# Kernel optimization log

Measured on AMD Instinct MI355X. Metric: run time of the kernel, lower is better.

## Reference

```python
import jax, jax.numpy as jnp
import numpy as np

RADIUS = 4
SIGMA_1 = 5.0
SIGMA_2 = 1.0


def _gaussian_kernel(dtype):
    # norm.pdf(d)/norm.pdf(0) == exp(-d^2/2)
    x2 = jnp.linspace(-RADIUS, RADIUS, 2 * RADIUS + 1) ** 2
    dist = jnp.sqrt(x2[:, None] + x2[None, :]) / SIGMA_1
    return jnp.exp(-0.5 * dist ** 2).astype(dtype)  # [k, k]


def setup_inputs() -> dict:
    key = jax.random.key(0)
    k1, k2 = jax.random.split(key)
    labels = jax.random.uniform(k1, (16, 20, 256, 256), dtype=jnp.float32)
    inputs = jax.random.uniform(k2, (16, 3, 256, 256), dtype=jnp.float32)
    return {"labels": labels, "inputs": inputs}


def reference(labels, inputs):
    B, K, H, W = labels.shape
    kernel = _gaussian_kernel(labels.dtype)

    # per-class mean color: mean(inputs * probs, HW) / (mean(probs, HW) + 1e-5)
    pmean = jnp.mean(labels, axis=(2, 3))                           # [B, K]
    xmean = jnp.einsum('bchw,bkhw->bkc', inputs, labels) / (H * W)  # [B, K, C]
    class_mean = xmean / (pmean[..., None] + 1e-5)                  # [B, K, C]

    # diff = sum_c (x_c - m_c)^2, expanded to avoid a [B,K,C,H,W] intermediate
    x2sum = jnp.sum(inputs ** 2, axis=1)                            # [B, H, W]
    cross = jnp.einsum('bchw,bkc->bkhw', inputs, class_mean)        # [B, K, H, W]
    m2 = jnp.sum(class_mean ** 2, axis=-1)                          # [B, K]
    diff = x2sum[:, None] - 2.0 * cross + m2[:, :, None, None]      # [B, K, H, W]
    weights = jnp.exp(-(diff ** 2) / (SIGMA_2 ** 2))                # [B, K, H, W]

    def blur(x):  # single-channel gaussian conv, vectorized over B*K
        lhs = x.reshape(B * K, 1, H, W)
        rhs = kernel[None, None]  # [1, 1, k, k]
        y = jax.lax.conv_general_dilated(
            lhs, rhs, window_strides=(1, 1),
            padding=[(RADIUS, RADIUS), (RADIUS, RADIUS)],
            dimension_numbers=('NCHW', 'OIHW', 'NCHW'))
        return y.reshape(B, K, H, W)

    num = jnp.sum(labels * blur(labels * weights), axis=(0, 2, 3))  # [K]
    den = jnp.sum(labels * blur(weights), axis=(0, 2, 3))           # [K]
    loss = jnp.sum(jnp.abs(num / (den + 1e-6)))
    return jnp.asarray(K, labels.dtype) - loss
```

## Files before the change

kernel.cpp:

```cpp
#include <hip/hip_runtime.h>

#define B_ 16
#define K_ 20
#define H_ 256
#define W_ 256
#define HW_ (H_*W_)
#define BK_ (B_*K_)
#define TH_ 64
#define BATCH_ 8
#define KT_ 10
#define SCH_ 16
#define NBLK_FUSED_ (4*K_*B_)

#define WS_ND_   (SCH_*4*BK_)
#define WS_CNT_  (WS_ND_ + 2*NBLK_FUSED_)

#define G1T 0.980198673f
#define G2T 0.923116346f
#define G3T 0.835270211f
#define G4T 0.726149037f

__device__ __forceinline__ float rfl(float v) {
    return __int_as_float(__builtin_amdgcn_readfirstlane(__float_as_int(v)));
}

__global__ __launch_bounds__(256) void stats_k(const float* __restrict__ labels,
                                               const float* __restrict__ inputs,
                                               float* __restrict__ ws) {
    const int x = threadIdx.x;
    const int chunk = blockIdx.x;
    const int kt = blockIdx.y;
    const int b  = blockIdx.z;
    const int k0 = kt * KT_;
    if (chunk == 0 && kt == 0 && b == 0 && x == 0)
        ((unsigned*)(ws + WS_CNT_))[0] = 0u;

    const int cbase = chunk * (16 * W_ / 4);
    const float4* in0 = (const float4*)inputs + (size_t)b * 3 * (HW_/4) + cbase;
    const float4* in1 = in0 + (HW_/4);
    const float4* in2 = in1 + (HW_/4);
    const float4* lb  = (const float4*)labels + (size_t)(b * K_ + k0) * (HW_/4) + cbase;

    float acc[KT_][4];
#pragma unroll
    for (int kk = 0; kk < KT_; ++kk)
        acc[kk][0] = acc[kk][1] = acc[kk][2] = acc[kk][3] = 0.f;

#pragma unroll
    for (int it = 0; it < 4; ++it) {
        const int idx = it * 256 + x;
        const float4 a0 = in0[idx];
        const float4 a1 = in1[idx];
        const float4 a2 = in2[idx];
#pragma unroll
        for (int kk = 0; kk < KT_; ++kk) {
            const float4 l = lb[kk * (HW_/4) + idx];
            acc[kk][0] += (l.x + l.y) + (l.z + l.w);
            acc[kk][1] += fmaf(l.w, a0.w, fmaf(l.z, a0.z, fmaf(l.y, a0.y, l.x * a0.x)));
            acc[kk][2] += fmaf(l.w, a1.w, fmaf(l.z, a1.z, fmaf(l.y, a1.y, l.x * a1.x)));
            acc[kk][3] += fmaf(l.w, a2.w, fmaf(l.z, a2.z, fmaf(l.y, a2.y, l.x * a2.x)));
        }
    }

#pragma unroll
    for (int kk = 0; kk < KT_; ++kk)
#pragma unroll
        for (int q = 0; q < 4; ++q)
            for (int o = 32; o > 0; o >>= 1)
                acc[kk][q] += __shfl_down(acc[kk][q], o);

    __shared__ float sred[4][KT_][4];
    const int widx = x >> 6, lane = x & 63;
    if (lane == 0)
#pragma unroll
        for (int kk = 0; kk < KT_; ++kk)
#pragma unroll
            for (int q = 0; q < 4; ++q) sred[widx][kk][q] = acc[kk][q];
    __syncthreads();
    if (x < KT_ * 4) {
        const int kk = x >> 2, q = x & 3;
        const float v = sred[0][kk][q] + sred[1][kk][q] + sred[2][kk][q] + sred[3][kk][q];
        ws[(chunk * 4 + q) * BK_ + b * K_ + k0 + kk] = v;
    }
}

#define CAT(m) (((m) < 8) ? ring[(m)&7] : PL[(m)&7])

__global__ __launch_bounds__(256) void fused_k(const float* __restrict__ labels,
                                               const float* __restrict__ inputs,
                                               float* __restrict__ ws,
                                               float* __restrict__ out) {
    const int x = threadIdx.x;
    const int bid = blockIdx.x;
    const int swz = (bid & 7) * (NBLK_FUSED_ / 8) + (bid >> 3);
    const int b   = swz / (4 * K_);
    const int rem = swz - b * (4 * K_);
    const int k   = rem >> 2;
    const int sg  = rem & 3;
    const int bk  = b * K_ + k;
    const int r0  = sg * TH_;

    float s0 = 0.f, s1 = 0.f, s2 = 0.f, s3 = 0.f;
#pragma unroll
    for (int c = 0; c < SCH_; ++c) {
        const float* p = ws + c * 4 * BK_;
        s0 += p[bk]; s1 += p[BK_ + bk]; s2 += p[2*BK_ + bk]; s3 += p[3*BK_ + bk];
    }
    const float dnv = s0 + 1e-5f * (float)HW_;
    const float c0 = s1 / dnv, c1 = s2 / dnv, c2 = s3 / dnv;
    const float tc0 = rfl(2.f * c0), tc1 = rfl(2.f * c1), tc2 = rfl(2.f * c2);
    const float m2v = rfl(c0*c0 + c1*c1 + c2*c2);

    const float* lb  = labels + (size_t)bk * HW_;
    const float* i0p = inputs + (size_t)b * 3 * HW_;
    const float* i1p = i0p + HW_;
    const float* i2p = i1p + HW_;

    __shared__ float2 sv[2][BATCH_/2][W_ + 8];
    if (x < 64) {
        const int bu = x >> 5, j2 = (x >> 3) & 3, p = x & 7;
        const int col = (p < 4) ? p : (W_ + p);
        sv[bu][j2][col] = make_float2(0.f, 0.f);
    }

    float ring[8], PL[8], PW[8];
#pragma unroll
    for (int i = 0; i < 8; ++i) {
        const int gr = r0 - 4 + i;
        ring[i] = (gr >= 0) ? lb[gr * W_ + x] : 0.f;
    }
#pragma unroll
    for (int i = 0; i < 8; ++i)
        PL[i] = lb[(r0 + 4 + i) * W_ + x];
#pragma unroll
    for (int i = 0; i < 8; ++i) {
        const int r = r0 + i;
        const float a0 = i0p[r * W_ + x], a1 = i1p[r * W_ + x], a2 = i2p[r * W_ + x];
        const float d = fmaf(a0, a0 - tc0, fmaf(a1, a1 - tc1, fmaf(a2, a2 - tc2, m2v)));
        PW[i] = __expf(-d * d);
    }
    __syncthreads();

    float num = 0.f, den = 0.f;
#pragma unroll 1
    for (int bt = 0; bt < TH_ / BATCH_; ++bt) {
        const int R = r0 + bt * BATCH_;
        const int bf = bt & 1;
        float NL[8];
#pragma unroll
        for (int i = 0; i < 8; ++i) {
            const int gr = R + 12 + i;
            NL[i] = (gr < H_) ? lb[gr * W_ + x] : 0.f;
        }
        float a0v[8], a1v[8], a2v[8];
#pragma unroll
        for (int i = 0; i < 8; ++i) {
            int r = R + 8 + i; r = (r < H_) ? r : H_ - 1;
            a0v[i] = i0p[r * W_ + x]; a1v[i] = i1p[r * W_ + x]; a2v[i] = i2p[r * W_ + x];
        }
#pragma unroll
        for (int j2 = 0; j2 < 4; ++j2) {
            const int j = 2 * j2;
            const float v0 = fmaf(G4T, CAT(j) + CAT(j+8),
                             fmaf(G3T, CAT(j+1) + CAT(j+7),
                             fmaf(G2T, CAT(j+2) + CAT(j+6),
                             fmaf(G1T, CAT(j+3) + CAT(j+5), CAT(j+4)))));
            const float v1 = fmaf(G4T, CAT(j+1) + CAT(j+9),
                             fmaf(G3T, CAT(j+2) + CAT(j+8),
                             fmaf(G2T, CAT(j+3) + CAT(j+7),
                             fmaf(G1T, CAT(j+4) + CAT(j+6), CAT(j+5)))));
            sv[bf][j2][4 + x] = make_float2(v0, v1);
        }
        asm volatile("s_waitcnt lgkmcnt(0)" ::: "memory");
        __builtin_amdgcn_s_barrier();
        asm volatile("" ::: "memory");
#pragma unroll
        for (int j2 = 0; j2 < 4; ++j2) {
            const int j = 2 * j2;
            const float2* s = &sv[bf][j2][x];
            const float2 t0 = s[0], t1 = s[1], t2 = s[2], t3 = s[3], t4 = s[4],
                         t5 = s[5], t6 = s[6], t7 = s[7], t8 = s[8];
            const float blx = fmaf(G4T, t0.x + t8.x,
                              fmaf(G3T, t1.x + t7.x,
                              fmaf(G2T, t2.x + t6.x,
                              fmaf(G1T, t3.x + t5.x, t4.x))));
            const float bly = fmaf(G4T, t0.y + t8.y,
                              fmaf(G3T, t1.y + t7.y,
                              fmaf(G2T, t2.y + t6.y,
                              fmaf(G1T, t3.y + t5.y, t4.y))));
            const float u0 = PW[j]   * blx;
            const float u1 = PW[j+1] * bly;
            den += u0 + u1;
            num = fmaf(CAT(j+4), u0, fmaf(CAT(j+5), u1, num));
        }
#pragma unroll
        for (int i = 0; i < 8; ++i) {
            const float d = fmaf(a0v[i], a0v[i] - tc0,
                            fmaf(a1v[i], a1v[i] - tc1,
                            fmaf(a2v[i], a2v[i] - tc2, m2v)));
            const float w = __expf(-d * d);
            ring[i] = PL[i]; PL[i] = NL[i]; PW[i] = w;
        }
    }

    const int widx = x >> 6, lane = x & 63;
    for (int o = 32; o > 0; o >>= 1) { num += __shfl_down(num, o); den += __shfl_down(den, o); }
    __shared__ float rb[4][2];
    __shared__ unsigned sdone;
    __syncthreads();
    if (lane == 0) { rb[widx][0] = num; rb[widx][1] = den; }
    __syncthreads();
    if (x == 0) {
        const float fn = rb[0][0] + rb[1][0] + rb[2][0] + rb[3][0];
        const float fd = rb[0][1] + rb[1][1] + rb[2][1] + rb[3][1];
        float2* nd2 = (float2*)(ws + WS_ND_);
        nd2[k * 64 + b * 4 + sg] = make_float2(fn, fd);
        __threadfence();
        sdone = atomicAdd((unsigned*)(ws + WS_CNT_), 1u);
    }
    __syncthreads();
    if (sdone == (unsigned)(NBLK_FUSED_ - 1)) {
        __threadfence();
        if (x < 64) {
            float term = 0.f;
            if (x < K_) {
                const float2* nd2 = (const float2*)(ws + WS_ND_);
                float ns = 0.f, ds = 0.f;
                for (int i = 0; i < 64; ++i) {
                    const float2 v = nd2[x * 64 + i];
                    ns += v.x; ds += v.y;
                }
                term = fabsf(ns / (ds + 1e-6f));
            }
            for (int o = 32; o > 0; o >>= 1) term += __shfl_down(term, o);
            if (x == 0) out[0] = (float)K_ - term;
        }
    }
}

extern "C" void kernel_launch(void* const* d_in, const int* in_sizes, int n_in,
                              void* d_out, int out_size, void* d_ws, size_t ws_size,
                              hipStream_t stream) {
    const float* labels = (const float*)d_in[0];
    const float* inputs = (const float*)d_in[1];
    float* ws = (float*)d_ws;

    stats_k<<<dim3(SCH_, K_ / KT_, B_), 256, 0, stream>>>(labels, inputs, ws);
    fused_k<<<NBLK_FUSED_, 256, 0, stream>>>(labels, inputs, ws, (float*)d_out);
}
```

Before: 203.0 us.

## Tile fused kernel by 8-row strips over 10 classes, reusing inputs from shared memory

The fused kernel now gives each block an 8-row strip and a half of the classes (10), instead of a 64-row strip of a single class. The input pixels and their squared norm are staged once in shared memory and reused across the 10 classes, and the per-class numerator and denominator go into global accumulators via float atomics. The aim is to stop re-reading the 3-channel inputs for every class. The cost is a 4-row halo on each side of every 8-row strip, so label rows are over-read heavily (16 rows loaded per 8 computed), plus more barriers and atomic contention. The float atomics also make the summation order nondeterministic.

```diff
diff --git a/kernel.cpp b/kernel.cpp
--- a/kernel.cpp
+++ b/kernel.cpp
@@ -6,14 +6,14 @@
 #define W_ 256
 #define HW_ (H_*W_)
 #define BK_ (B_*K_)
-#define TH_ 64
-#define BATCH_ 8
+#define TH_ 8
 #define KT_ 10
 #define SCH_ 16
-#define NBLK_FUSED_ (4*K_*B_)
+#define NSTR_ 32
+#define NBLK_FUSED_ (B_*NSTR_*2)
 
 #define WS_ND_   (SCH_*4*BK_)
-#define WS_CNT_  (WS_ND_ + 2*NBLK_FUSED_)
+#define WS_CNT_  (WS_ND_ + 2*K_)
 
 #define G1T 0.980198673f
 #define G2T 0.923116346f
@@ -32,8 +32,8 @@
     const int kt = blockIdx.y;
     const int b  = blockIdx.z;
     const int k0 = kt * KT_;
-    if (chunk == 0 && kt == 0 && b == 0 && x == 0)
-        ((unsigned*)(ws + WS_CNT_))[0] = 0u;
+    if (chunk == 0 && kt == 0 && b == 0 && x < 2*K_ + 1)
+        ws[WS_ND_ + x] = 0.f;
 
     const int cbase = chunk * (16 * W_ / 4);
     const float4* in0 = (const float4*)inputs + (size_t)b * 3 * (HW_/4) + cbase;
@@ -84,100 +84,94 @@
     }
 }
 
-#define CAT(m) (((m) < 8) ? ring[(m)&7] : PL[(m)&7])
-
 __global__ __launch_bounds__(256) void fused_k(const float* __restrict__ labels,
                                                const float* __restrict__ inputs,
                                                float* __restrict__ ws,
                                                float* __restrict__ out) {
     const int x = threadIdx.x;
+    const int lane = x & 63, widx = x >> 6;
     const int bid = blockIdx.x;
     const int swz = (bid & 7) * (NBLK_FUSED_ / 8) + (bid >> 3);
-    const int b   = swz / (4 * K_);
-    const int rem = swz - b * (4 * K_);
-    const int k   = rem >> 2;
-    const int sg  = rem & 3;
-    const int bk  = b * K_ + k;
+    const int b   = swz >> 6;
+    const int rem = swz & 63;
+    const int sg  = rem >> 1;
+    const int kh  = rem & 1;
     const int r0  = sg * TH_;
-
-    float s0 = 0.f, s1 = 0.f, s2 = 0.f, s3 = 0.f;
-#pragma unroll
-    for (int c = 0; c < SCH_; ++c) {
-        const float* p = ws + c * 4 * BK_;
-        s0 += p[bk]; s1 += p[BK_ + bk]; s2 += p[2*BK_ + bk]; s3 += p[3*BK_ + bk];
-    }
-    const float dnv = s0 + 1e-5f * (float)HW_;
-    const float c0 = s1 / dnv, c1 = s2 / dnv, c2 = s3 / dnv;
-    const float tc0 = rfl(2.f * c0), tc1 = rfl(2.f * c1), tc2 = rfl(2.f * c2);
-    const float m2v = rfl(c0*c0 + c1*c1 + c2*c2);
-
-    const float* lb  = labels + (size_t)bk * HW_;
+    const int k0g = kh * KT_;
+
     const float* i0p = inputs + (size_t)b * 3 * HW_;
     const float* i1p = i0p + HW_;
     const float* i2p = i1p + HW_;
 
-    __shared__ float2 sv[2][BATCH_/2][W_ + 8];
-    if (x < 64) {
-        const int bu = x >> 5, j2 = (x >> 3) & 3, p = x & 7;
+    __shared__ float4 si[TH_][W_];
+    __shared__ float2 sv[TH_/2][W_ + 8];
+    __shared__ float rb[2][4][2];
+    __shared__ unsigned sdone;
+
+    if (x < 32) {
+        const int j2 = x >> 3, p = x & 7;
         const int col = (p < 4) ? p : (W_ + p);
-        sv[bu][j2][col] = make_float2(0.f, 0.f);
-    }
-
-    float ring[8], PL[8], PW[8];
-#pragma unroll
-    for (int i = 0; i < 8; ++i) {
+        sv[j2][col] = make_float2(0.f, 0.f);
+    }
+
+#pragma unroll
+    for (int j = 0; j < TH_; ++j) {
+        const int r = r0 + j;
+        const float a0 = i0p[r * W_ + x], a1 = i1p[r * W_ + x], a2 = i2p[r * W_ + x];
+        si[j][x] = make_float4(a0, a1, a2, fmaf(a0, a0, fmaf(a1, a1, a2 * a2)));
+    }
+
+    const float* lb = labels + (size_t)(b * K_ + k0g) * HW_;
+    float L[16], NL[16];
+#pragma unroll
+    for (int i = 0; i < 16; ++i) {
         const int gr = r0 - 4 + i;
-        ring[i] = (gr >= 0) ? lb[gr * W_ + x] : 0.f;
-    }
-#pragma unroll
-    for (int i = 0; i < 8; ++i)
-        PL[i] = lb[(r0 + 4 + i) * W_ + x];
-#pragma unroll
-    for (int i = 0; i < 8; ++i) {
-        const int r = r0 + i;
-        const float a0 = i0p[r * W_ + x], a1 = i1p[r * W_ + x], a2 = i2p[r * W_ + x];
-        const float d = fmaf(a0, a0 - tc0, fmaf(a1, a1 - tc1, fmaf(a2, a2 - tc2, m2v)));
-        PW[i] = __expf(-d * d);
-    }
-    __syncthreads();
-
-    float num = 0.f, den = 0.f;
+        L[i] = (gr >= 0 && gr < H_) ? lb[gr * W_ + x] : 0.f;
+    }
+
+    __syncthreads();
+
 #pragma unroll 1
-    for (int bt = 0; bt < TH_ / BATCH_; ++bt) {
-        const int R = r0 + bt * BATCH_;
-        const int bf = bt & 1;
-        float NL[8];
-#pragma unroll
-        for (int i = 0; i < 8; ++i) {
-            const int gr = R + 12 + i;
-            NL[i] = (gr < H_) ? lb[gr * W_ + x] : 0.f;
-        }
-        float a0v[8], a1v[8], a2v[8];
-#pragma unroll
-        for (int i = 0; i < 8; ++i) {
-            int r = R + 8 + i; r = (r < H_) ? r : H_ - 1;
-            a0v[i] = i0p[r * W_ + x]; a1v[i] = i1p[r * W_ + x]; a2v[i] = i2p[r * W_ + x];
-        }
-#pragma unroll
-        for (int j2 = 0; j2 < 4; ++j2) {
+    for (int kk = 0; kk < KT_; ++kk) {
+        const int bk = b * K_ + k0g + kk;
+        float s0 = 0.f, s1 = 0.f, s2 = 0.f, s3 = 0.f;
+#pragma unroll
+        for (int c = 0; c < SCH_; ++c) {
+            const float* p = ws + c * 4 * BK_;
+            s0 += p[bk]; s1 += p[BK_ + bk]; s2 += p[2*BK_ + bk]; s3 += p[3*BK_ + bk];
+        }
+        const float dnv = s0 + 1e-5f * (float)HW_;
+        const float c0 = s1 / dnv, c1 = s2 / dnv, c2 = s3 / dnv;
+        const float tc0 = rfl(2.f * c0), tc1 = rfl(2.f * c1), tc2 = rfl(2.f * c2);
+        const float m2v = rfl(c0*c0 + c1*c1 + c2*c2);
+
+        if (kk < KT_ - 1) {
+#pragma unroll
+            for (int i = 0; i < 16; ++i) {
+                const int gr = r0 - 4 + i;
+                NL[i] = (gr >= 0 && gr < H_) ? lb[HW_ + gr * W_ + x] : 0.f;
+            }
+        }
+#pragma unroll
+        for (int j2 = 0; j2 < TH_/2; ++j2) {
             const int j = 2 * j2;
-            const float v0 = fmaf(G4T, CAT(j) + CAT(j+8),
-                             fmaf(G3T, CAT(j+1) + CAT(j+7),
-                             fmaf(G2T, CAT(j+2) + CAT(j+6),
-                             fmaf(G1T, CAT(j+3) + CAT(j+5), CAT(j+4)))));
-            const float v1 = fmaf(G4T, CAT(j+1) + CAT(j+9),
-                             fmaf(G3T, CAT(j+2) + CAT(j+8),
-                             fmaf(G2T, CAT(j+3) + CAT(j+7),
-                             fmaf(G1T, CAT(j+4) + CAT(j+6), CAT(j+5)))));
-            sv[bf][j2][4 + x] = make_float2(v0, v1);
+            const float v0 = fmaf(G4T, L[j]   + L[j+8],
+                             fmaf(G3T, L[j+1] + L[j+7],
+                             fmaf(G2T, L[j+2] + L[j+6],
+                             fmaf(G1T, L[j+3] + L[j+5], L[j+4]))));
+            const float v1 = fmaf(G4T, L[j+1] + L[j+9],
+                             fmaf(G3T, L[j+2] + L[j+8],
+                             fmaf(G2T, L[j+3] + L[j+7],
+                             fmaf(G1T, L[j+4] + L[j+6], L[j+5]))));
+            sv[j2][4 + x] = make_float2(v0, v1);
         }
         asm volatile("s_waitcnt lgkmcnt(0)" ::: "memory");
         __builtin_amdgcn_s_barrier();
         asm volatile("" ::: "memory");
-#pragma unroll
-        for (int j2 = 0; j2 < 4; ++j2) {
-            const int j = 2 * j2;
-            const float2* s = &sv[bf][j2][x];
+        float num = 0.f, den = 0.f;
+#pragma unroll
+        for (int j2 = 0; j2 < TH_/2; ++j2) {
+            const float2* s = &sv[j2][x];
             const float2 t0 = s[0], t1 = s[1], t2 = s[2], t3 = s[3], t4 = s[4],
                          t5 = s[5], t6 = s[6], t7 = s[7], t8 = s[8];
             const float blx = fmaf(G4T, t0.x + t8.x,
@@ -188,33 +182,36 @@
                               fmaf(G3T, t1.y + t7.y,
                               fmaf(G2T, t2.y + t6.y,
                               fmaf(G1T, t3.y + t5.y, t4.y))));
-            const float u0 = PW[j]   * blx;
-            const float u1 = PW[j+1] * bly;
+            const float4 iv0 = si[2*j2][x];
+            const float4 iv1 = si[2*j2+1][x];
+            const float d0 = fmaf(-iv0.x, tc0, fmaf(-iv0.y, tc1, fmaf(-iv0.z, tc2, iv0.w + m2v)));
+            const float d1 = fmaf(-iv1.x, tc0, fmaf(-iv1.y, tc1, fmaf(-iv1.z, tc2, iv1.w + m2v)));
+            const float u0 = __expf(-d0 * d0) * blx;
+            const float u1 = __expf(-d1 * d1) * bly;
             den += u0 + u1;
-            num = fmaf(CAT(j+4), u0, fmaf(CAT(j+5), u1, num));
-        }
-#pragma unroll
-        for (int i = 0; i < 8; ++i) {
-            const float d = fmaf(a0v[i], a0v[i] - tc0,
-                            fmaf(a1v[i], a1v[i] - tc1,
-                            fmaf(a2v[i], a2v[i] - tc2, m2v)));
-            const float w = __expf(-d * d);
-            ring[i] = PL[i]; PL[i] = NL[i]; PW[i] = w;
-        }
-    }
-
-    const int widx = x >> 6, lane = x & 63;
-    for (int o = 32; o > 0; o >>= 1) { num += __shfl_down(num, o); den += __shfl_down(den, o); }
-    __shared__ float rb[4][2];
-    __shared__ unsigned sdone;
-    __syncthreads();
-    if (lane == 0) { rb[widx][0] = num; rb[widx][1] = den; }
+            num = fmaf(L[2*j2+4], u0, fmaf(L[2*j2+5], u1, num));
+        }
+        for (int o = 32; o > 0; o >>= 1) { num += __shfl_down(num, o); den += __shfl_down(den, o); }
+        if (lane == 0) { rb[kk & 1][widx][0] = num; rb[kk & 1][widx][1] = den; }
+        asm volatile("s_waitcnt lgkmcnt(0)" ::: "memory");
+        __builtin_amdgcn_s_barrier();
+        asm volatile("" ::: "memory");
+        if (x == 0) {
+            const int p = kk & 1;
+            const float fn = rb[p][0][0] + rb[p][1][0] + rb[p][2][0] + rb[p][3][0];
+            const float fd = rb[p][0][1] + rb[p][1][1] + rb[p][2][1] + rb[p][3][1];
+            atomicAdd(&ws[WS_ND_ + 2*(k0g + kk)],     fn);
+            atomicAdd(&ws[WS_ND_ + 2*(k0g + kk) + 1], fd);
+        }
+        if (kk < KT_ - 1) {
+#pragma unroll
+            for (int i = 0; i < 16; ++i) L[i] = NL[i];
+            lb += HW_;
+        }
+    }
+
     __syncthreads();
     if (x == 0) {
-        const float fn = rb[0][0] + rb[1][0] + rb[2][0] + rb[3][0];
-        const float fd = rb[0][1] + rb[1][1] + rb[2][1] + rb[3][1];
-        float2* nd2 = (float2*)(ws + WS_ND_);
-        nd2[k * 64 + b * 4 + sg] = make_float2(fn, fd);
         __threadfence();
         sdone = atomicAdd((unsigned*)(ws + WS_CNT_), 1u);
     }
@@ -224,12 +221,8 @@
         if (x < 64) {
             float term = 0.f;
             if (x < K_) {
-                const float2* nd2 = (const float2*)(ws + WS_ND_);
-                float ns = 0.f, ds = 0.f;
-                for (int i = 0; i < 64; ++i) {
-                    const float2 v = nd2[x * 64 + i];
-                    ns += v.x; ds += v.y;
-                }
+                const float ns = ws[WS_ND_ + 2*x];
+                const float ds = ws[WS_ND_ + 2*x + 1];
                 term = fabsf(ns / (ds + 1e-6f));
             }
             for (int o = 32; o > 0; o >>= 1) term += __shfl_down(term, o);
```

Result: slower. 288.7 us (+42.2%).
